# Kernel optimization log

Hardware: AMD Instinct MI355X
Metric: run time of the kernel (lower is better)

## Reference

```python
import jax, jax.numpy as jnp
import numpy as np
import math

B, T, H, NH, BLOCK = 2, 2048, 1024, 16, 2048
HS = H // NH  # 64, even as required by RoPE


def make_rope_cache(hs, block):
    # positions t = 1..block (note: source starts at 1, not 0)
    t = np.arange(1, block + 1, dtype=np.float32)[:, None]          # (block, 1)
    i = np.arange(1, hs // 2 + 1, dtype=np.float32)[None, :]        # (1, hs/2)
    theta = (1.0 / 10000.0) ** (2.0 * (i - 1.0) / hs)               # (1, hs/2)
    ang = t * theta                                                  # (block, hs/2)
    return jnp.asarray(np.stack([np.cos(ang), np.sin(ang)], axis=-1))  # (block, hs/2, 2)


def setup_inputs() -> dict:
    key = jax.random.key(0)
    ks = jax.random.split(key, 10)
    s = 0.02
    x = jax.random.normal(ks[0], (B, T, H), jnp.float32)
    masks = jax.random.randint(ks[1], (B, T), 0, 2, jnp.int32)  # 1 = padding token
    Wq = jax.random.normal(ks[2], (H, H), jnp.float32) * s
    bq = jnp.zeros((H,), jnp.float32)
    Wk = jax.random.normal(ks[3], (H, H), jnp.float32) * s
    bk = jnp.zeros((H,), jnp.float32)
    Wv = jax.random.normal(ks[4], (H, H), jnp.float32) * s
    bv = jnp.zeros((H,), jnp.float32)
    Wo = jax.random.normal(ks[5], (H, H), jnp.float32) * s  # final_proj, no bias
    rope = make_rope_cache(HS, BLOCK)
    return {"x": x, "masks": masks, "Wq": Wq, "bq": bq, "Wk": Wk, "bk": bk,
            "Wv": Wv, "bv": bv, "Wo": Wo, "rope": rope}


def _apply_rope(x, cos, sin):
    # x: (B, nh, T, hs); cos/sin: (T, hs/2) broadcast over (B, nh)
    xe, xo = x[..., ::2], x[..., 1::2]
    real = cos * xe - sin * xo
    imag = sin * xe + cos * xo
    return jnp.stack([real, imag], axis=-1).reshape(x.shape)


def reference(x, masks, Wq, bq, Wk, bk, Wv, bv, Wo, rope):
    Bn, Tn, Hn = x.shape
    nh, hs = NH, Hn // NH

    def proj(W, b):
        # torch Linear: x @ W.T + b -> (B, nh, T, hs)
        return (x @ W.T + b).reshape(Bn, Tn, nh, hs).transpose(0, 2, 1, 3)

    Q, K, V = proj(Wq, bq), proj(Wk, bk), proj(Wv, bv)
    cos, sin = rope[:Tn, :, 0], rope[:Tn, :, 1]
    Q = _apply_rope(Q, cos, sin)
    K = _apply_rope(K, cos, sin)

    att = jnp.einsum('bhqd,bhkd->bhqk', Q, K) * (1.0 / math.sqrt(hs))
    causal = jnp.tril(jnp.ones((Tn, Tn), bool))
    att = jnp.where(causal[None, None, :, :], att, -1e10)          # causal mask
    att = jnp.where((masks == 1)[:, None, None, :], -1e10, att)   # padding mask on keys
    att = jax.nn.softmax(att, axis=-1)

    y = jnp.einsum('bhqk,bhkd->bhqd', att, V)
    y = y.transpose(0, 2, 1, 3).reshape(Bn, Tn, Hn)
    return y @ Wo.T  # final_proj has no bias
```

## Files before the change

### kernel.cpp

```cpp
#include <hip/hip_runtime.h>

typedef short short8 __attribute__((ext_vector_type(8)));
typedef float floatx4 __attribute__((ext_vector_type(4)));
typedef unsigned short u16;
typedef unsigned long long u64;

#define Tn 2048
#define Kdim 1024
#define QSCALE 0.18033688011112042f
#define FIXEDMAX 20.0f

__device__ inline u16 f2bf(float x) {
    union { float f; unsigned u; } c; c.f = x;
    unsigned u = c.u;
    u += 0x7fffu + ((u >> 16) & 1u);
    return (u16)(u >> 16);
}
__device__ inline float bf2f(u16 h) {
    union { unsigned u; float f; } c; c.u = ((unsigned)h) << 16;
    return c.f;
}
__device__ inline floatx4 mfma16(short8 a, short8 b, floatx4 c) {
    return __builtin_amdgcn_mfma_f32_16x16x32_bf16(a, b, c, 0, 0, 0);
}
__device__ inline void async16(const void* g, void* l) {
    __builtin_amdgcn_global_load_lds((const __attribute__((address_space(1))) void*)g,
                                     (__attribute__((address_space(3))) void*)l, 16, 0, 0);
}

__global__ __launch_bounds__(256) void cvt_all_k(
    const float* __restrict__ x, const float* __restrict__ wq, const float* __restrict__ wk,
    const float* __restrict__ wv, const float* __restrict__ wo, u16* __restrict__ dst)
{
    int i = blockIdx.x * 256 + threadIdx.x;
    const float* s; int off;
    if (i < 1048576) { s = x; off = i; }
    else {
        int j = i - 1048576; int seg = j >> 18; off = j & 262143;
        s = (seg == 0) ? wq : (seg == 1) ? wk : (seg == 2) ? wv : wo;
    }
    float4 v = ((const float4*)s)[off];
    u64 pk = (u64)f2bf(v.x) | ((u64)f2bf(v.y) << 16) | ((u64)f2bf(v.z) << 32) | ((u64)f2bf(v.w) << 48);
    ((u64*)dst)[i] = pk;
}

__global__ __launch_bounds__(256, 3) void gemm_qkv_k(
    const u16* __restrict__ A,
    const u16* __restrict__ W0, const u16* __restrict__ W1, const u16* __restrict__ W2,
    const float* __restrict__ b0, const float* __restrict__ b1, const float* __restrict__ b2,
    u16* o0, u16* o1, u16* o2,
    const float2* __restrict__ rope)
{
    int z = blockIdx.z;
    const u16* W = (z == 0) ? W0 : (z == 1 ? W1 : W2);
    const float* bias = (z == 0) ? b0 : (z == 1 ? b1 : b2);
    u16* outp = (z == 0) ? o0 : (z == 1 ? o1 : o2);

    __shared__ __align__(16) char lds[32768];
    int tid = threadIdx.x;
    int w = tid >> 6, lane = tid & 63, quad = lane >> 4, l15 = lane & 15;
    int m0 = blockIdx.y * 128, n0 = blockIdx.x * 128;
    int wm = w * 32;

    floatx4 acc[2][8];
    floatx4 vzero = {0.f, 0.f, 0.f, 0.f};
#pragma unroll
    for (int i = 0; i < 2; ++i)
#pragma unroll
        for (int j = 0; j < 8; ++j) acc[i][j] = vzero;

    for (int k0 = 0; k0 < Kdim; k0 += 64) {
#pragma unroll
        for (int j = 0; j < 4; ++j) {
            int f = j * 256 + tid, r = f >> 3, c = (f & 7) ^ (r & 7);
            async16(A + (size_t)(m0 + r) * Kdim + k0 + c * 8, lds + j * 4096 + w * 1024);
            async16(W + (size_t)(n0 + r) * Kdim + k0 + c * 8, lds + 16384 + j * 4096 + w * 1024);
        }
        __syncthreads();
        short8 af[2][2];
#pragma unroll
        for (int mt = 0; mt < 2; ++mt) {
            int ra = wm + mt * 16 + l15;
            const char* pa = lds + ra * 128;
#pragma unroll
            for (int ks = 0; ks < 2; ++ks)
                af[mt][ks] = *(const short8*)(pa + (((ks * 4 + quad) ^ (ra & 7)) << 4));
        }
#pragma unroll
        for (int ks = 0; ks < 2; ++ks)
#pragma unroll
            for (int nt = 0; nt < 8; ++nt) {
                int rb = nt * 16 + l15;
                short8 bf = *(const short8*)(lds + 16384 + rb * 128 + (((ks * 4 + quad) ^ (rb & 7)) << 4));
                acc[0][nt] = mfma16(af[0][ks], bf, acc[0][nt]);
                acc[1][nt] = mfma16(af[1][ks], bf, acc[1][nt]);
            }
        __syncthreads();
    }

    int mbase = m0 + wm;
    if (z <= 1) {
        float osc = (z == 0) ? QSCALE : 1.0f;
#pragma unroll
        for (int nt = 0; nt < 8; ++nt) {
            int col = n0 + nt * 16 + l15;
            float bv = bias[col];
            int p = (col & 63) >> 1;
#pragma unroll
            for (int mt = 0; mt < 2; ++mt) {
                floatx4 a = acc[mt][nt];
#pragma unroll
                for (int r = 0; r < 4; ++r) {
                    int row = mbase + mt * 16 + quad * 4 + r;
                    float v = a[r] + bv;
                    float ov = __shfl_xor(v, 1, 64);
                    float2 cs = rope[(row & (Tn - 1)) * 32 + p];
                    float res = (cs.x * v + ((lane & 1) ? cs.y * ov : -cs.y * ov)) * osc;
                    float pres = __shfl_xor(res, 1, 64);
                    if (!(lane & 1)) {
                        unsigned pk = (unsigned)f2bf(res) | ((unsigned)f2bf(pres) << 16);
                        *(unsigned*)(outp + (size_t)row * 1024 + col) = pk;
                    }
                }
            }
        }
    } else {
#pragma unroll
        for (int nt = 0; nt < 8; ++nt) {
            int col = n0 + nt * 16 + l15;
            float bv = bias[col];
#pragma unroll
            for (int mt = 0; mt < 2; ++mt) {
                floatx4 a = acc[mt][nt];
                int row0 = mbase + mt * 16 + quad * 4;
                int bb = row0 >> 11, t0 = row0 & (Tn - 1);
                u64 pk = (u64)f2bf(a[0] + bv) | ((u64)f2bf(a[1] + bv) << 16)
                       | ((u64)f2bf(a[2] + bv) << 32) | ((u64)f2bf(a[3] + bv) << 48);
                *(u64*)(outp + (size_t)(bb * 1024 + col) * Tn + t0) = pk;
            }
        }
    }
}

__global__ __launch_bounds__(256, 5) void gemm_o_k(
    const u16* __restrict__ A, const u16* __restrict__ W, float* __restrict__ out)
{
    __shared__ __align__(16) char lds[24576];
    int tid = threadIdx.x;
    int w = tid >> 6, lane = tid & 63, quad = lane >> 4, l15 = lane & 15;
    int m0 = blockIdx.y * 128, n0 = blockIdx.x * 64;
    int wm = w * 32;

    floatx4 acc[2][4];
    floatx4 vzero = {0.f, 0.f, 0.f, 0.f};
#pragma unroll
    for (int i = 0; i < 2; ++i)
#pragma unroll
        for (int j = 0; j < 4; ++j) acc[i][j] = vzero;

    for (int k0 = 0; k0 < Kdim; k0 += 64) {
#pragma unroll
        for (int j = 0; j < 4; ++j) {
            int f = j * 256 + tid, r = f >> 3, c = (f & 7) ^ (r & 7);
            async16(A + (size_t)(m0 + r) * Kdim + k0 + c * 8, lds + j * 4096 + w * 1024);
        }
#pragma unroll
        for (int j = 0; j < 2; ++j) {
            int f = j * 256 + tid, r = f >> 3, c = (f & 7) ^ (r & 7);
            async16(W + (size_t)(n0 + r) * Kdim + k0 + c * 8, lds + 16384 + j * 4096 + w * 1024);
        }
        __syncthreads();
        short8 af[2][2];
#pragma unroll
        for (int mt = 0; mt < 2; ++mt) {
            int ra = wm + mt * 16 + l15;
            const char* pa = lds + ra * 128;
#pragma unroll
            for (int ks = 0; ks < 2; ++ks)
                af[mt][ks] = *(const short8*)(pa + (((ks * 4 + quad) ^ (ra & 7)) << 4));
        }
#pragma unroll
        for (int ks = 0; ks < 2; ++ks)
#pragma unroll
            for (int nt = 0; nt < 4; ++nt) {
                int rb = nt * 16 + l15;
                short8 bf = *(const short8*)(lds + 16384 + rb * 128 + (((ks * 4 + quad) ^ (rb & 7)) << 4));
                acc[0][nt] = mfma16(af[0][ks], bf, acc[0][nt]);
                acc[1][nt] = mfma16(af[1][ks], bf, acc[1][nt]);
            }
        __syncthreads();
    }

#pragma unroll
    for (int nt = 0; nt < 4; ++nt) {
        int col = n0 + nt * 16 + l15;
#pragma unroll
        for (int mt = 0; mt < 2; ++mt) {
            floatx4 a = acc[mt][nt];
#pragma unroll
            for (int r = 0; r < 4; ++r) {
                int row = m0 + wm + mt * 16 + quad * 4 + r;
                out[(size_t)row * 1024 + col] = a[r];
            }
        }
    }
}

__global__ __launch_bounds__(64) void vmean_k(const u16* __restrict__ Vt, float* __restrict__ vmean) {
    int row = blockIdx.x;
    int lane = threadIdx.x;
    const u16* p = Vt + (size_t)row * Tn;
    float s = 0.f;
    for (int i = lane * 8; i < Tn; i += 512) {
        short8 v = *(const short8*)(p + i);
#pragma unroll
        for (int j = 0; j < 8; ++j) s += bf2f((u16)v[j]);
    }
#pragma unroll
    for (int off = 1; off < 64; off <<= 1) s += __shfl_xor(s, off, 64);
    if (lane == 0) vmean[row] = s * (1.f / 2048.f);
}

__global__ __launch_bounds__(256) void flash_k(
    const u16* __restrict__ Qb, const u16* __restrict__ Kb, const u16* __restrict__ Vt,
    const int* __restrict__ masks, const float* __restrict__ vmean, u16* __restrict__ Yb)
{
    int bid = blockIdx.x;
    int bh = (bid & 7) * 4 + ((bid >> 3) & 3);
    int qt = 31 - (bid >> 5);
    int b = bh >> 4, h = bh & 15;
    int tid = threadIdx.x, w = tid >> 6, lane = tid & 63, quad = lane >> 4, l15 = lane & 15;
    int sc = (lane & 7) ^ (lane >> 3);

    __shared__ __align__(16) u16 ldsK[2][64 * 64];
    __shared__ __align__(16) u16 ldsV[2][64 * 64];
    __shared__ __align__(16) u16 ldsP[4][16 * 64];

    int ktiles = qt + 1;
    unsigned blo = 0, bhi = 0;
    for (int j = 0; j < ktiles; ++j) {
        u64 mk = __ballot(masks[b * Tn + j * 64 + lane] != 0);
        if (lane == j) { blo = (unsigned)mk; bhi = (unsigned)(mk >> 32); }
    }

    auto stage = [&](int bb, int k0) {
#pragma unroll
        for (int j = 0; j < 2; ++j) {
            int row = j * 32 + w * 8 + (lane >> 3);
            const u16* gk = Kb + (size_t)(b * Tn + k0 + row) * 1024 + h * 64 + sc * 8;
            async16(gk, (char*)&ldsK[bb][0] + (j * 32 + w * 8) * 128);
            const u16* gv = Vt + (size_t)(b * 1024 + h * 64 + row) * Tn + k0 + sc * 8;
            async16(gv, (char*)&ldsV[bb][0] + (j * 32 + w * 8) * 128);
        }
    };
    floatx4 vzero = {0.f, 0.f, 0.f, 0.f};

    int q0 = qt * 64 + w * 16;
    short8 qf[2];
    {
        const u16* qp = Qb + (size_t)(b * Tn + q0 + l15) * 1024 + h * 64 + quad * 8;
        qf[0] = *(const short8*)qp;
        qf[1] = *(const short8*)(qp + 32);
    }
    floatx4 o[4];
    float lsum = 0.f;
#pragma unroll
    for (int i = 0; i < 4; ++i) o[i] = vzero;

    int sh0 = quad * 4;
    char* pb = (char*)&ldsP[w][0] + l15 * 128 + ((quad & 1) << 3);

    stage(0, 0);
    for (int kt = 0; kt < ktiles; ++kt) {
        int k0 = kt * 64;
        int bb = kt & 1;
        __syncthreads();

        short8 kf[4][2], vf[4][2];
#pragma unroll
        for (int f = 0; f < 4; ++f) {
            int key = f * 16 + l15;
            const char* kbase = (const char*)&ldsK[bb][0] + key * 128;
            const char* vbase = (const char*)&ldsV[bb][0] + key * 128;
#pragma unroll
            for (int ks = 0; ks < 2; ++ks) {
                int slot = ((quad + ks * 4) ^ (key & 7)) << 4;
                kf[f][ks] = *(const short8*)(kbase + slot);
                vf[f][ks] = *(const short8*)(vbase + slot);
            }
        }
        if (kt + 1 < ktiles) stage(bb ^ 1, k0 + 64);

        unsigned mlo = __shfl(blo, kt, 64), mhi = __shfl(bhi, kt, 64);
        floatx4 ci[4];
        if (k0 + 63 <= q0) {
#pragma unroll
            for (int f = 0; f < 4; ++f) {
                unsigned nf = (((f & 2) ? mhi : mlo) >> (((f & 1) << 4) + sh0)) & 0xFu;
#pragma unroll
                for (int r = 0; r < 4; ++r)
                    ci[f][r] = ((nf >> r) & 1u) ? -1e10f : -FIXEDMAX;
            }
        } else {
            int dqb = q0 + l15 - k0 - sh0;
#pragma unroll
            for (int f = 0; f < 4; ++f) {
                unsigned nf = (((f & 2) ? mhi : mlo) >> (((f & 1) << 4) + sh0)) & 0xFu;
                int dq = dqb - f * 16;
#pragma unroll
                for (int r = 0; r < 4; ++r)
                    ci[f][r] = (((nf >> r) & 1u) || (r > dq)) ? -1e10f : -FIXEDMAX;
            }
        }

        floatx4 s[4];
#pragma unroll
        for (int f = 0; f < 4; ++f) {
            s[f] = mfma16(kf[f][0], qf[0], ci[f]);
            s[f] = mfma16(kf[f][1], qf[1], s[f]);
        }

#pragma unroll
        for (int f = 0; f < 4; ++f) {
            float p0 = __builtin_amdgcn_exp2f(s[f][0]);
            float p1 = __builtin_amdgcn_exp2f(s[f][1]);
            float p2 = __builtin_amdgcn_exp2f(s[f][2]);
            float p3 = __builtin_amdgcn_exp2f(s[f][3]);
            lsum += (p0 + p1) + (p2 + p3);
            unsigned pka, pkb;
            asm("v_cvt_pk_bf16_f32 %0, %1, %2" : "=v"(pka) : "v"(p0), "v"(p1));
            asm("v_cvt_pk_bf16_f32 %0, %1, %2" : "=v"(pkb) : "v"(p2), "v"(p3));
            u64 pk = (u64)pka | ((u64)pkb << 32);
            *(u64*)(pb + (((f * 2 + (quad >> 1)) ^ (l15 & 7)) << 4)) = pk;
        }
        __asm__ volatile("s_waitcnt lgkmcnt(0)" ::: "memory");
        short8 pf0 = *(const short8*)((const char*)&ldsP[w][0] + l15 * 128 + ((quad ^ (l15 & 7)) << 4));
        short8 pf1 = *(const short8*)((const char*)&ldsP[w][0] + l15 * 128 + (((quad + 4) ^ (l15 & 7)) << 4));
#pragma unroll
        for (int nb = 0; nb < 4; ++nb) {
            o[nb] = mfma16(pf0, vf[nb][0], o[nb]);
            o[nb] = mfma16(pf1, vf[nb][1], o[nb]);
        }
    }

    lsum += __shfl_xor(lsum, 16, 64);
    lsum += __shfl_xor(lsum, 32, 64);

#pragma unroll
    for (int r = 0; r < 4; ++r) {
        int qq = q0 + quad * 4 + r;
        float l = __shfl(lsum, quad * 4 + r, 64);
        bool degen = (l == 0.f);
        float linv = 1.0f / l;
#pragma unroll
        for (int nb = 0; nb < 4; ++nb) {
            int d = nb * 16 + l15;
            float val = degen ? vmean[b * 1024 + h * 64 + d] : o[nb][r] * linv;
            float pv = __shfl_xor(val, 1, 64);
            if (!(lane & 1)) {
                unsigned pk = (unsigned)f2bf(val) | ((unsigned)f2bf(pv) << 16);
                *(unsigned*)(Yb + (size_t)(b * Tn + qq) * 1024 + h * 64 + d) = pk;
            }
        }
    }
}

extern "C" void kernel_launch(void* const* d_in, const int* in_sizes, int n_in,
                              void* d_out, int out_size, void* d_ws, size_t ws_size,
                              hipStream_t stream) {
    const float* x  = (const float*)d_in[0];
    const int* masks = (const int*)d_in[1];
    const float* Wq = (const float*)d_in[2];
    const float* bq = (const float*)d_in[3];
    const float* Wk = (const float*)d_in[4];
    const float* bk = (const float*)d_in[5];
    const float* Wv = (const float*)d_in[6];
    const float* bv = (const float*)d_in[7];
    const float* Wo = (const float*)d_in[8];
    const float2* rope = (const float2*)d_in[9];
    float* out = (float*)d_out;

    char* ws = (char*)d_ws;
    u16* xb   = (u16*)(ws);
    u16* Wqb  = (u16*)(ws + (8  << 20));
    u16* Wkb  = (u16*)(ws + (10 << 20));
    u16* Wvb  = (u16*)(ws + (12 << 20));
    u16* Wob  = (u16*)(ws + (14 << 20));
    u16* Qb   = (u16*)(ws + (16 << 20));
    u16* Kb2  = (u16*)(ws + (24 << 20));
    u16* Vt   = (u16*)(ws + (32 << 20));
    u16* Yb   = (u16*)(ws + (40 << 20));
    float* vm = (float*)(ws + (48 << 20));

    cvt_all_k<<<8192, 256, 0, stream>>>(x, Wq, Wk, Wv, Wo, xb);

    gemm_qkv_k<<<dim3(8, 32, 3), 256, 0, stream>>>(xb, Wqb, Wkb, Wvb, bq, bk, bv,
                                                   Qb, Kb2, Vt, rope);
    vmean_k<<<2048, 64, 0, stream>>>(Vt, vm);
    flash_k<<<1024, 256, 0, stream>>>(Qb, Kb2, Vt, masks, vm, Yb);
    gemm_o_k<<<dim3(16, 32), 256, 0, stream>>>(Yb, Wob, out);
}
```

Measured before the change: 199.5 us.

## Split long causal query tiles across key ranges with atomic combine, shrink GEMM tiles

The longest half of the query tiles in the flash kernel now have their key range split across two blocks. Each block accumulates unnormalized O and row sums into fp32 buffers with atomics, and a new combine kernel normalizes the result and writes the bf16 Y. The cvt kernel also zeroes these buffers, and the QKV and output GEMMs get smaller tiles to launch more blocks. This is meant to balance causal work and raise occupancy, at the cost of extra fp32 atomic traffic and an extra kernel launch. It relies on a fixed max (FIXEDMAX) rather than a running max for the partial sums, and the flash K/V staging loses its double buffering.

```diff
diff --git a/kernel.cpp b/kernel.cpp
--- a/kernel.cpp
+++ b/kernel.cpp
@@ -30,9 +30,18 @@
 
 __global__ __launch_bounds__(256) void cvt_all_k(
     const float* __restrict__ x, const float* __restrict__ wq, const float* __restrict__ wk,
-    const float* __restrict__ wv, const float* __restrict__ wo, u16* __restrict__ dst)
+    const float* __restrict__ wv, const float* __restrict__ wo, u16* __restrict__ dst,
+    float4* __restrict__ o32z, float4* __restrict__ l32z)
 {
-    int i = blockIdx.x * 256 + threadIdx.x;
+    int bx = blockIdx.x;
+    if (bx >= 8192) {
+        int j = (bx - 8192) * 256 + threadIdx.x;
+        float4 z = {0.f, 0.f, 0.f, 0.f};
+        if (bx < 12288) o32z[j] = z;
+        else l32z[j - 1048576] = z;
+        return;
+    }
+    int i = bx * 256 + threadIdx.x;
     const float* s; int off;
     if (i < 1048576) { s = x; off = i; }
     else {
@@ -44,7 +53,7 @@
     ((u64*)dst)[i] = pk;
 }
 
-__global__ __launch_bounds__(256, 3) void gemm_qkv_k(
+__global__ __launch_bounds__(256, 5) void gemm_qkv_k(
     const u16* __restrict__ A,
     const u16* __restrict__ W0, const u16* __restrict__ W1, const u16* __restrict__ W2,
     const float* __restrict__ b0, const float* __restrict__ b1, const float* __restrict__ b2,
@@ -56,24 +65,28 @@
     const float* bias = (z == 0) ? b0 : (z == 1 ? b1 : b2);
     u16* outp = (z == 0) ? o0 : (z == 1 ? o1 : o2);
 
-    __shared__ __align__(16) char lds[32768];
+    __shared__ __align__(16) char lds[24576];
     int tid = threadIdx.x;
     int w = tid >> 6, lane = tid & 63, quad = lane >> 4, l15 = lane & 15;
-    int m0 = blockIdx.y * 128, n0 = blockIdx.x * 128;
+    int m0 = blockIdx.y * 128, n0 = blockIdx.x * 64;
     int wm = w * 32;
 
-    floatx4 acc[2][8];
+    floatx4 acc[2][4];
     floatx4 vzero = {0.f, 0.f, 0.f, 0.f};
 #pragma unroll
     for (int i = 0; i < 2; ++i)
 #pragma unroll
-        for (int j = 0; j < 8; ++j) acc[i][j] = vzero;
+        for (int j = 0; j < 4; ++j) acc[i][j] = vzero;
 
     for (int k0 = 0; k0 < Kdim; k0 += 64) {
 #pragma unroll
         for (int j = 0; j < 4; ++j) {
             int f = j * 256 + tid, r = f >> 3, c = (f & 7) ^ (r & 7);
             async16(A + (size_t)(m0 + r) * Kdim + k0 + c * 8, lds + j * 4096 + w * 1024);
+        }
+#pragma unroll
+        for (int j = 0; j < 2; ++j) {
+            int f = j * 256 + tid, r = f >> 3, c = (f & 7) ^ (r & 7);
             async16(W + (size_t)(n0 + r) * Kdim + k0 + c * 8, lds + 16384 + j * 4096 + w * 1024);
         }
         __syncthreads();
@@ -89,7 +102,7 @@
 #pragma unroll
         for (int ks = 0; ks < 2; ++ks)
 #pragma unroll
-            for (int nt = 0; nt < 8; ++nt) {
+            for (int nt = 0; nt < 4; ++nt) {
                 int rb = nt * 16 + l15;
                 short8 bf = *(const short8*)(lds + 16384 + rb * 128 + (((ks * 4 + quad) ^ (rb & 7)) << 4));
                 acc[0][nt] = mfma16(af[0][ks], bf, acc[0][nt]);
@@ -102,7 +115,7 @@
     if (z <= 1) {
         float osc = (z == 0) ? QSCALE : 1.0f;
 #pragma unroll
-        for (int nt = 0; nt < 8; ++nt) {
+        for (int nt = 0; nt < 4; ++nt) {
             int col = n0 + nt * 16 + l15;
             float bv = bias[col];
             int p = (col & 63) >> 1;
@@ -126,7 +139,7 @@
         }
     } else {
 #pragma unroll
-        for (int nt = 0; nt < 8; ++nt) {
+        for (int nt = 0; nt < 4; ++nt) {
             int col = n0 + nt * 16 + l15;
             float bv = bias[col];
 #pragma unroll
@@ -142,32 +155,28 @@
     }
 }
 
-__global__ __launch_bounds__(256, 5) void gemm_o_k(
+__global__ __launch_bounds__(256, 4) void gemm_o_k(
     const u16* __restrict__ A, const u16* __restrict__ W, float* __restrict__ out)
 {
-    __shared__ __align__(16) char lds[24576];
+    __shared__ __align__(16) char lds[16384];
     int tid = threadIdx.x;
     int w = tid >> 6, lane = tid & 63, quad = lane >> 4, l15 = lane & 15;
-    int m0 = blockIdx.y * 128, n0 = blockIdx.x * 64;
-    int wm = w * 32;
-
-    floatx4 acc[2][4];
+    int m0 = blockIdx.y * 64, n0 = blockIdx.x * 64;
+    int wm = (w >> 1) * 32, wn = (w & 1) * 32;
+
+    floatx4 acc[2][2];
     floatx4 vzero = {0.f, 0.f, 0.f, 0.f};
 #pragma unroll
     for (int i = 0; i < 2; ++i)
 #pragma unroll
-        for (int j = 0; j < 4; ++j) acc[i][j] = vzero;
+        for (int j = 0; j < 2; ++j) acc[i][j] = vzero;
 
     for (int k0 = 0; k0 < Kdim; k0 += 64) {
 #pragma unroll
-        for (int j = 0; j < 4; ++j) {
+        for (int j = 0; j < 2; ++j) {
             int f = j * 256 + tid, r = f >> 3, c = (f & 7) ^ (r & 7);
             async16(A + (size_t)(m0 + r) * Kdim + k0 + c * 8, lds + j * 4096 + w * 1024);
-        }
-#pragma unroll
-        for (int j = 0; j < 2; ++j) {
-            int f = j * 256 + tid, r = f >> 3, c = (f & 7) ^ (r & 7);
-            async16(W + (size_t)(n0 + r) * Kdim + k0 + c * 8, lds + 16384 + j * 4096 + w * 1024);
+            async16(W + (size_t)(n0 + r) * Kdim + k0 + c * 8, lds + 8192 + j * 4096 + w * 1024);
         }
         __syncthreads();
         short8 af[2][2];
@@ -182,9 +191,9 @@
 #pragma unroll
         for (int ks = 0; ks < 2; ++ks)
 #pragma unroll
-            for (int nt = 0; nt < 4; ++nt) {
-                int rb = nt * 16 + l15;
-                short8 bf = *(const short8*)(lds + 16384 + rb * 128 + (((ks * 4 + quad) ^ (rb & 7)) << 4));
+            for (int nt = 0; nt < 2; ++nt) {
+                int rb = wn + nt * 16 + l15;
+                short8 bf = *(const short8*)(lds + 8192 + rb * 128 + (((ks * 4 + quad) ^ (rb & 7)) << 4));
                 acc[0][nt] = mfma16(af[0][ks], bf, acc[0][nt]);
                 acc[1][nt] = mfma16(af[1][ks], bf, acc[1][nt]);
             }
@@ -192,8 +201,8 @@
     }
 
 #pragma unroll
-    for (int nt = 0; nt < 4; ++nt) {
-        int col = n0 + nt * 16 + l15;
+    for (int nt = 0; nt < 2; ++nt) {
+        int col = n0 + wn + nt * 16 + l15;
 #pragma unroll
         for (int mt = 0; mt < 2; ++mt) {
             floatx4 a = acc[mt][nt];
@@ -223,34 +232,41 @@
 
 __global__ __launch_bounds__(256) void flash_k(
     const u16* __restrict__ Qb, const u16* __restrict__ Kb, const u16* __restrict__ Vt,
-    const int* __restrict__ masks, const float* __restrict__ vmean, u16* __restrict__ Yb)
+    const int* __restrict__ masks, float* __restrict__ O32, float* __restrict__ L32)
 {
     int bid = blockIdx.x;
     int bh = (bid & 7) * 4 + ((bid >> 3) & 3);
-    int qt = 31 - (bid >> 5);
+    int idx = bid >> 5;
+    int qt, kt0, kt1;
+    if (idx < 32) {
+        qt = 31 - (idx >> 1);
+        int half = (qt + 2) >> 1;
+        if (idx & 1) { kt0 = half; kt1 = qt + 1; } else { kt0 = 0; kt1 = half; }
+    } else {
+        qt = 47 - idx; kt0 = 0; kt1 = qt + 1;
+    }
     int b = bh >> 4, h = bh & 15;
     int tid = threadIdx.x, w = tid >> 6, lane = tid & 63, quad = lane >> 4, l15 = lane & 15;
     int sc = (lane & 7) ^ (lane >> 3);
 
-    __shared__ __align__(16) u16 ldsK[2][64 * 64];
-    __shared__ __align__(16) u16 ldsV[2][64 * 64];
+    __shared__ __align__(16) u16 ldsK[64 * 64];
+    __shared__ __align__(16) u16 ldsV[64 * 64];
     __shared__ __align__(16) u16 ldsP[4][16 * 64];
 
-    int ktiles = qt + 1;
     unsigned blo = 0, bhi = 0;
-    for (int j = 0; j < ktiles; ++j) {
+    for (int j = kt0; j < kt1; ++j) {
         u64 mk = __ballot(masks[b * Tn + j * 64 + lane] != 0);
         if (lane == j) { blo = (unsigned)mk; bhi = (unsigned)(mk >> 32); }
     }
 
-    auto stage = [&](int bb, int k0) {
+    auto stage = [&](int k0) {
 #pragma unroll
         for (int j = 0; j < 2; ++j) {
             int row = j * 32 + w * 8 + (lane >> 3);
             const u16* gk = Kb + (size_t)(b * Tn + k0 + row) * 1024 + h * 64 + sc * 8;
-            async16(gk, (char*)&ldsK[bb][0] + (j * 32 + w * 8) * 128);
+            async16(gk, (char*)ldsK + (j * 32 + w * 8) * 128);
             const u16* gv = Vt + (size_t)(b * 1024 + h * 64 + row) * Tn + k0 + sc * 8;
-            async16(gv, (char*)&ldsV[bb][0] + (j * 32 + w * 8) * 128);
+            async16(gv, (char*)ldsV + (j * 32 + w * 8) * 128);
         }
     };
     floatx4 vzero = {0.f, 0.f, 0.f, 0.f};
@@ -270,18 +286,17 @@
     int sh0 = quad * 4;
     char* pb = (char*)&ldsP[w][0] + l15 * 128 + ((quad & 1) << 3);
 
-    stage(0, 0);
-    for (int kt = 0; kt < ktiles; ++kt) {
+    stage(kt0 * 64);
+    for (int kt = kt0; kt < kt1; ++kt) {
         int k0 = kt * 64;
-        int bb = kt & 1;
         __syncthreads();
 
         short8 kf[4][2], vf[4][2];
 #pragma unroll
         for (int f = 0; f < 4; ++f) {
             int key = f * 16 + l15;
-            const char* kbase = (const char*)&ldsK[bb][0] + key * 128;
-            const char* vbase = (const char*)&ldsV[bb][0] + key * 128;
+            const char* kbase = (const char*)ldsK + key * 128;
+            const char* vbase = (const char*)ldsV + key * 128;
 #pragma unroll
             for (int ks = 0; ks < 2; ++ks) {
                 int slot = ((quad + ks * 4) ^ (key & 7)) << 4;
@@ -289,7 +304,8 @@
                 vf[f][ks] = *(const short8*)(vbase + slot);
             }
         }
-        if (kt + 1 < ktiles) stage(bb ^ 1, k0 + 64);
+        __syncthreads();
+        if (kt + 1 < kt1) stage(k0 + 64);
 
         unsigned mlo = __shfl(blo, kt, 64), mhi = __shfl(bhi, kt, 64);
         floatx4 ci[4];
@@ -345,24 +361,36 @@
 
     lsum += __shfl_xor(lsum, 16, 64);
     lsum += __shfl_xor(lsum, 32, 64);
-
-#pragma unroll
-    for (int r = 0; r < 4; ++r) {
-        int qq = q0 + quad * 4 + r;
-        float l = __shfl(lsum, quad * 4 + r, 64);
-        bool degen = (l == 0.f);
-        float linv = 1.0f / l;
-#pragma unroll
-        for (int nb = 0; nb < 4; ++nb) {
-            int d = nb * 16 + l15;
-            float val = degen ? vmean[b * 1024 + h * 64 + d] : o[nb][r] * linv;
-            float pv = __shfl_xor(val, 1, 64);
-            if (!(lane & 1)) {
-                unsigned pk = (unsigned)f2bf(val) | ((unsigned)f2bf(pv) << 16);
-                *(unsigned*)(Yb + (size_t)(b * Tn + qq) * 1024 + h * 64 + d) = pk;
-            }
-        }
-    }
+    if (quad == 0) atomicAdd(&L32[(b * 16 + h) * 2048 + q0 + l15], lsum);
+
+    float* obase = O32 + (size_t)(b * Tn + q0 + quad * 4) * 1024 + h * 64 + l15;
+#pragma unroll
+    for (int r = 0; r < 4; ++r)
+#pragma unroll
+        for (int nb = 0; nb < 4; ++nb)
+            atomicAdd(obase + (size_t)r * 1024 + nb * 16, o[nb][r]);
+}
+
+__global__ __launch_bounds__(256) void combine_k(
+    const float4* __restrict__ O32, const float* __restrict__ L32,
+    const float* __restrict__ vmean, u16* __restrict__ Yb)
+{
+    int row = blockIdx.x;
+    int b = row >> 11, t = row & 2047;
+    int tid = threadIdx.x;
+    int d = tid * 4;
+    float l = L32[(b * 16 + (d >> 6)) * 2048 + t];
+    float4 ov = O32[(size_t)row * 256 + tid];
+    float v0, v1, v2, v3;
+    if (l == 0.f) {
+        const float* vp = vmean + b * 1024 + d;
+        v0 = vp[0]; v1 = vp[1]; v2 = vp[2]; v3 = vp[3];
+    } else {
+        float inv = 1.0f / l;
+        v0 = ov.x * inv; v1 = ov.y * inv; v2 = ov.z * inv; v3 = ov.w * inv;
+    }
+    u64 pk = (u64)f2bf(v0) | ((u64)f2bf(v1) << 16) | ((u64)f2bf(v2) << 32) | ((u64)f2bf(v3) << 48);
+    ((u64*)Yb)[(size_t)row * 256 + tid] = pk;
 }
 
 extern "C" void kernel_launch(void* const* d_in, const int* in_sizes, int n_in,
@@ -391,12 +419,15 @@
     u16* Vt   = (u16*)(ws + (32 << 20));
     u16* Yb   = (u16*)(ws + (40 << 20));
     float* vm = (float*)(ws + (48 << 20));
-
-    cvt_all_k<<<8192, 256, 0, stream>>>(x, Wq, Wk, Wv, Wo, xb);
-
-    gemm_qkv_k<<<dim3(8, 32, 3), 256, 0, stream>>>(xb, Wqb, Wkb, Wvb, bq, bk, bv,
-                                                   Qb, Kb2, Vt, rope);
+    float* O32 = (float*)(ws + (49 << 20));
+    float* L32 = (float*)(ws + (65 << 20));
+
+    cvt_all_k<<<12352, 256, 0, stream>>>(x, Wq, Wk, Wv, Wo, xb, (float4*)O32, (float4*)L32);
+
+    gemm_qkv_k<<<dim3(16, 32, 3), 256, 0, stream>>>(xb, Wqb, Wkb, Wvb, bq, bk, bv,
+                                                    Qb, Kb2, Vt, rope);
     vmean_k<<<2048, 64, 0, stream>>>(Vt, vm);
-    flash_k<<<1024, 256, 0, stream>>>(Qb, Kb2, Vt, masks, vm, Yb);
-    gemm_o_k<<<dim3(16, 32), 256, 0, stream>>>(Yb, Wob, out);
-}
+    flash_k<<<1536, 256, 0, stream>>>(Qb, Kb2, Vt, masks, O32, L32);
+    combine_k<<<4096, 256, 0, stream>>>((const float4*)O32, L32, vm, Yb);
+    gemm_o_k<<<dim3(16, 64), 256, 0, stream>>>(Yb, Wob, out);
+}
```

After: 209.6 us. 1.05x slower.
